# Optimization experiments

Measured on AMD Instinct MI355X. Metric: run time of the kernel, lower is better.

## Reference

```python
import jax, jax.numpy as jnp
import numpy as np

T, H, W, C, HD, K = 4, 128, 128, 256, 8, 9
F = C // HD


def setup_inputs() -> dict:
    key = jax.random.key(0)
    ks = jax.random.split(key, 6)
    x = jax.random.normal(ks[0], (T, H, W, C), jnp.float32)
    attn = jax.random.uniform(ks[1], (1, HD, T, H, W, K), jnp.float32)
    attn = attn / attn.sum(-1, keepdims=True)  # softmax-normalized neighbor weights
    # integer flow offsets (dt, dh, dw) in [-3, 3], as produced by non-local search
    flows = jax.random.randint(ks[2], (1, HD, T, H, W, K, 3), -3, 4, jnp.int32)
    v_w = jax.random.normal(ks[3], (C, C), jnp.float32) * (C ** -0.5)
    proj_w = jax.random.normal(ks[4], (C, C), jnp.float32) * (C ** -0.5)
    proj_b = jnp.zeros((C,), jnp.float32)
    return dict(x=x, attn=attn, flows=flows, v_w=v_w, proj_w=proj_w, proj_b=proj_b)


def reference(x, attn, flows, v_w, proj_w, proj_b):
    T, H, W, C = x.shape
    HD = attn.shape[1]
    F = C // HD
    # v projection, split heads: [T,H,W,HD,F]
    v = (x @ v_w.T).reshape(T, H, W, HD, F)
    fl = flows[0]  # [HD,T,H,W,K,3] integer offsets (dt, dh, dw)
    tt = jnp.clip(jnp.arange(T)[None, :, None, None, None] + fl[..., 0], 0, T - 1)
    hh = jnp.clip(jnp.arange(H)[None, None, :, None, None] + fl[..., 1], 0, H - 1)
    ww = jnp.clip(jnp.arange(W)[None, None, None, :, None] + fl[..., 2], 0, W - 1)
    hd = jnp.arange(HD)[:, None, None, None, None]
    # flow-guided non-local gather: [HD,T,H,W,K,F]
    gathered = v[tt, hh, ww, hd]
    # attention-weighted sum over K neighbors, merge heads: [T,H,W,C]
    out = jnp.einsum('dthwk,dthwkf->thwdf', attn[0], gathered).reshape(T, H, W, C)
    # output projection
    return out @ proj_w.T + proj_b
```

## Files before the change

kernel.cpp:

```cpp
#include <hip/hip_runtime.h>
#include <hip/hip_bf16.h>

namespace {

constexpr int T = 4, H = 128, W = 128, C = 256, HD = 8, K = 9, F = 32;
constexpr int M = T * H * W;

typedef __attribute__((ext_vector_type(8))) short short8v;
typedef __attribute__((ext_vector_type(4))) float f32x4;

__device__ __forceinline__ unsigned short f2bf(float f) {
  unsigned u = __float_as_uint(f);
  unsigned r = (u + 0x7fffu + ((u >> 16) & 1u)) >> 16;
  return (unsigned short)r;
}

__device__ __forceinline__ float bf2f(unsigned short u) {
  return __uint_as_float(((unsigned)u) << 16);
}

template <int ALAYOUT, bool OUT_F32>
__global__ __launch_bounds__(256) void mfma_gemm(
    const void* __restrict__ Aptr, const float* __restrict__ Bw,
    void* __restrict__ Cptr, const float* __restrict__ bias) {
  __shared__ unsigned short As[128][40];
  __shared__ unsigned short Bs[128][40];
  const int m0 = blockIdx.x * 128;
  const int n0 = blockIdx.y * 128;
  const int t = threadIdx.x;
  const int lane = t & 63;
  const int wid = t >> 6;
  const int wm = wid >> 1, wn = wid & 1;
  const int fr = lane & 15;
  const int kg = lane >> 4;

  f32x4 acc[4][4];
#pragma unroll
  for (int ni = 0; ni < 4; ++ni) {
    float b = 0.f;
    if (OUT_F32) b = bias[n0 + wn * 64 + ni * 16 + fr];
#pragma unroll
    for (int mi = 0; mi < 4; ++mi) {
      acc[mi][ni][0] = b; acc[mi][ni][1] = b;
      acc[mi][ni][2] = b; acc[mi][ni][3] = b;
    }
  }

  for (int k0 = 0; k0 < C; k0 += 32) {
    __syncthreads();
    if (ALAYOUT == 2) {
      const unsigned short* Ab = (const unsigned short*)Aptr;
      const size_t hb = (size_t)(k0 >> 5) * M * 32;
#pragma unroll
      for (int i = 0; i < 2; ++i) {
        const int flat = t + i * 256;
        const int row = flat >> 2, kc = (flat & 3) * 8;
        *(short8v*)&As[row][kc] =
            *(const short8v*)(Ab + hb + (size_t)(m0 + row) * 32 + kc);
      }
    } else {
      const float* Af = (const float*)Aptr;
#pragma unroll
      for (int i = 0; i < 4; ++i) {
        const int flat = t + i * 256;
        const int row = flat >> 3, kc = (flat & 7) * 4;
        const float4 v4 = *(const float4*)(Af + (size_t)(m0 + row) * C + k0 + kc);
        ushort4 o;
        o.x = f2bf(v4.x); o.y = f2bf(v4.y); o.z = f2bf(v4.z); o.w = f2bf(v4.w);
        *(ushort4*)&As[row][kc] = o;
      }
    }
#pragma unroll
    for (int i = 0; i < 4; ++i) {
      const int flat = t + i * 256;
      const int row = flat >> 3, kc = (flat & 7) * 4;
      const float4 v4 = *(const float4*)(Bw + (size_t)(n0 + row) * C + k0 + kc);
      ushort4 o;
      o.x = f2bf(v4.x); o.y = f2bf(v4.y); o.z = f2bf(v4.z); o.w = f2bf(v4.w);
      *(ushort4*)&Bs[row][kc] = o;
    }
    __syncthreads();
    short8v af[4], bfv[4];
#pragma unroll
    for (int mi = 0; mi < 4; ++mi)
      af[mi] = *(const short8v*)&As[wm * 64 + mi * 16 + fr][kg * 8];
#pragma unroll
    for (int ni = 0; ni < 4; ++ni)
      bfv[ni] = *(const short8v*)&Bs[wn * 64 + ni * 16 + fr][kg * 8];
#pragma unroll
    for (int mi = 0; mi < 4; ++mi)
#pragma unroll
      for (int ni = 0; ni < 4; ++ni)
        acc[mi][ni] = __builtin_amdgcn_mfma_f32_16x16x32_bf16(
            af[mi], bfv[ni], acc[mi][ni], 0, 0, 0);
  }

#pragma unroll
  for (int mi = 0; mi < 4; ++mi) {
#pragma unroll
    for (int ni = 0; ni < 4; ++ni) {
      const int gcol = n0 + wn * 64 + ni * 16 + fr;
#pragma unroll
      for (int r = 0; r < 4; ++r) {
        const int grow = m0 + wm * 64 + mi * 16 + kg * 4 + r;
        if (OUT_F32) {
          ((float*)Cptr)[(size_t)grow * C + gcol] = acc[mi][ni][r];
        } else {
          ((unsigned short*)Cptr)[(size_t)grow * C + gcol] = f2bf(acc[mi][ni][r]);
        }
      }
    }
  }
}

struct __attribute__((packed, aligned(4))) I4p { int a, b, c, d; };
struct __attribute__((packed, aligned(4))) I2p { int a, b; };
struct __attribute__((packed, aligned(4))) F4p { float a, b, c, d; };

__global__ __launch_bounds__(256, 4) void gather_lds_kernel(
    const unsigned short* __restrict__ v, const float* __restrict__ attn,
    const int* __restrict__ flows, unsigned short* __restrict__ agg2) {
  __shared__ __align__(16) unsigned short halo[4 * 14 * 14 * 32];
  const int nb = (blockIdx.x & 7) * 256 + (blockIdx.x >> 3);
  const int head = nb & 7;
  const int tile = nb >> 3;
  const int h0 = (tile >> 4) * 8;
  const int w0 = (tile & 15) * 8;
  const int tid = threadIdx.x;
  const int s = tid & 63;
  const int tq = tid >> 6;
  const int h = h0 + (s >> 3);
  const int w = w0 + (s & 7);
  const int m = (tq << 14) | (h << 7) | w;

  const int base = ((head << 16) | m) * K;
  const int fb = base * 3;
  const I4p f0 = *(const I4p*)(flows + fb + 0);
  const I4p f1 = *(const I4p*)(flows + fb + 4);
  const I4p f2 = *(const I4p*)(flows + fb + 8);
  const I4p f3 = *(const I4p*)(flows + fb + 12);
  const I4p f4 = *(const I4p*)(flows + fb + 16);
  const I4p f5 = *(const I4p*)(flows + fb + 20);
  const I2p f6 = *(const I2p*)(flows + fb + 24);
  const int f7 = flows[fb + 26];
  const F4p a0 = *(const F4p*)(attn + base + 0);
  const F4p a1 = *(const F4p*)(attn + base + 4);
  const float a2 = attn[base + 8];

  const unsigned short* vhead = v + head * F;
  auto piece_src = [&](int pi, int& ldsoff) -> const short8v* {
    const int sliver = pi >> 2, j = pi & 3;
    const int tt = sliver / 196;
    const int rem = sliver - tt * 196;
    const int hh = rem / 14;
    const int ww = rem - hh * 14;
    const int hc = min(max(h0 - 3 + hh, 0), H - 1);
    const int wc = min(max(w0 - 3 + ww, 0), W - 1);
    const int sm = (tt << 14) | (hc << 7) | wc;
    ldsoff = sliver * 32 + (j ^ (sliver & 3)) * 8;
    return (const short8v*)(vhead + (size_t)sm * C + j * 8);
  };
  {
    short8v pc[7]; int lo[7];
#pragma unroll
    for (int it = 0; it < 7; ++it) pc[it] = *piece_src(tid + it * 256, lo[it]);
#pragma unroll
    for (int it = 0; it < 7; ++it) *(short8v*)&halo[lo[it]] = pc[it];
  }
  {
    short8v pc[5]; int lo[5];
#pragma unroll
    for (int it = 0; it < 5; ++it)
      pc[it] = *piece_src(1792 + tid + it * 256, lo[it]);
    short8v pt; int lot = 0;
    if (tid < 64) pt = *piece_src(3072 + tid, lot);
#pragma unroll
    for (int it = 0; it < 5; ++it) *(short8v*)&halo[lo[it]] = pc[it];
    if (tid < 64) *(short8v*)&halo[lot] = pt;
  }
  __syncthreads();

  const int d[27] = {f0.a, f0.b, f0.c, f0.d, f1.a, f1.b, f1.c, f1.d,
                     f2.a, f2.b, f2.c, f2.d, f3.a, f3.b, f3.c, f3.d,
                     f4.a, f4.b, f4.c, f4.d, f5.a, f5.b, f5.c, f5.d,
                     f6.a, f6.b, f7};
  const float aw[9] = {a0.a, a0.b, a0.c, a0.d, a1.a, a1.b, a1.c, a1.d, a2};
  int row[9];
#pragma unroll
  for (int k = 0; k < 9; ++k) {
    const int ts = min(max(tq + d[3 * k + 0], 0), T - 1);
    const int hs = min(max(h + d[3 * k + 1], 0), H - 1) - (h0 - 3);
    const int ws = min(max(w + d[3 * k + 2], 0), W - 1) - (w0 - 3);
    row[k] = (ts * 14 + hs) * 14 + ws;
  }

  float acc[32];
#pragma unroll
  for (int i = 0; i < 32; ++i) acc[i] = 0.f;
#pragma unroll
  for (int k = 0; k < 9; ++k) {
    const int rbase = row[k] * 32;
    const int rsw = row[k] & 3;
#pragma unroll
    for (int j = 0; j < 4; ++j) {
      const short8v p = *(const short8v*)&halo[rbase + (j ^ rsw) * 8];
#pragma unroll
      for (int e = 0; e < 8; ++e)
        acc[j * 8 + e] += aw[k] * bf2f((unsigned short)p[e]);
    }
  }

  unsigned short* dst = agg2 + ((size_t)head * M + m) * F;
#pragma unroll
  for (int j = 0; j < 4; ++j) {
    short8v o;
#pragma unroll
    for (int e = 0; e < 8; ++e) o[e] = (short)f2bf(acc[j * 8 + e]);
    *(short8v*)(dst + j * 8) = o;
  }
}

__global__ __launch_bounds__(256) void agg_proj_kernel(
    const unsigned short* __restrict__ v, const float* __restrict__ attn,
    const int* __restrict__ flows, const float* __restrict__ proj_w,
    const float* __restrict__ proj_b, float* __restrict__ out) {
  __shared__ float Agg[32][C];
  __shared__ float Bs[32][C];
  const int bid = blockIdx.x;
  const int t = bid >> 9;
  const int h0 = ((bid >> 5) & 15) * 8;
  const int w0 = (bid & 31) * 4;
  const int tid = threadIdx.x;

  const int g = tid >> 3;
  const int f4 = (tid & 7) * 4;
#pragma unroll
  for (int r = 0; r < 8; ++r) {
    const int pi = r * 32 + g;
    const int pos = pi >> 3;
    const int head = pi & 7;
    const int h = h0 + (pos >> 2);
    const int w = w0 + (pos & 3);
    const int base = (((head * T + t) * H + h) * W + w) * K;
    const int fbase = base * 3;
    float4 acc = {0.f, 0.f, 0.f, 0.f};
#pragma unroll
    for (int k = 0; k < K; ++k) {
      const int dt = flows[fbase + k * 3 + 0];
      const int dh = flows[fbase + k * 3 + 1];
      const int dw = flows[fbase + k * 3 + 2];
      const float aw = attn[base + k];
      const int tt = min(max(t + dt, 0), T - 1);
      const int hh = min(max(h + dh, 0), H - 1);
      const int ww = min(max(w + dw, 0), W - 1);
      const int mm = (tt * H + hh) * W + ww;
      const ushort4 r4 = *(const ushort4*)(v + (size_t)mm * C + head * F + f4);
      acc.x += aw * bf2f(r4.x);
      acc.y += aw * bf2f(r4.y);
      acc.z += aw * bf2f(r4.z);
      acc.w += aw * bf2f(r4.w);
    }
    *(float4*)&Agg[pos][head * F + f4] = acc;
  }
  __syncthreads();

  const int tx = tid & 31;
  const int ty = tid >> 5;
  float acc2[4][8];
  {
    const float4 b0 = *(const float4*)(proj_b + tx * 8);
    const float4 b1 = *(const float4*)(proj_b + tx * 8 + 4);
#pragma unroll
    for (int i = 0; i < 4; ++i) {
      acc2[i][0] = b0.x; acc2[i][1] = b0.y; acc2[i][2] = b0.z; acc2[i][3] = b0.w;
      acc2[i][4] = b1.x; acc2[i][5] = b1.y; acc2[i][6] = b1.z; acc2[i][7] = b1.w;
    }
  }
  for (int k0 = 0; k0 < C; k0 += 32) {
#pragma unroll
    for (int i = 0; i < 8; ++i) {
      const float4 w4 = *(const float4*)(proj_w + (size_t)tid * C + k0 + i * 4);
      Bs[i * 4 + 0][tid] = w4.x;
      Bs[i * 4 + 1][tid] = w4.y;
      Bs[i * 4 + 2][tid] = w4.z;
      Bs[i * 4 + 3][tid] = w4.w;
    }
    __syncthreads();
#pragma unroll 4
    for (int kk = 0; kk < 32; ++kk) {
      const float4 bb0 = *(const float4*)&Bs[kk][tx * 8];
      const float4 bb1 = *(const float4*)&Bs[kk][tx * 8 + 4];
      float a[4];
#pragma unroll
      for (int i = 0; i < 4; ++i) a[i] = Agg[ty * 4 + i][k0 + kk];
#pragma unroll
      for (int i = 0; i < 4; ++i) {
        acc2[i][0] += a[i] * bb0.x;
        acc2[i][1] += a[i] * bb0.y;
        acc2[i][2] += a[i] * bb0.z;
        acc2[i][3] += a[i] * bb0.w;
        acc2[i][4] += a[i] * bb1.x;
        acc2[i][5] += a[i] * bb1.y;
        acc2[i][6] += a[i] * bb1.z;
        acc2[i][7] += a[i] * bb1.w;
      }
    }
    __syncthreads();
  }
#pragma unroll
  for (int i = 0; i < 4; ++i) {
    const int pos = ty * 4 + i;
    const int h = h0 + (pos >> 2);
    const int w = w0 + (pos & 3);
    const int m = (t * H + h) * W + w;
    float4 o0, o1;
    o0.x = acc2[i][0]; o0.y = acc2[i][1]; o0.z = acc2[i][2]; o0.w = acc2[i][3];
    o1.x = acc2[i][4]; o1.y = acc2[i][5]; o1.z = acc2[i][6]; o1.w = acc2[i][7];
    *(float4*)(out + (size_t)m * C + tx * 8) = o0;
    *(float4*)(out + (size_t)m * C + tx * 8 + 4) = o1;
  }
}

}

extern "C" void kernel_launch(void* const* d_in, const int* in_sizes, int n_in,
                              void* d_out, int out_size, void* d_ws,
                              size_t ws_size, hipStream_t stream) {
  const float* x = (const float*)d_in[0];
  const float* attn = (const float*)d_in[1];
  const int* flows = (const int*)d_in[2];
  const float* v_w = (const float*)d_in[3];
  const float* proj_w = (const float*)d_in[4];
  const float* proj_b = (const float*)d_in[5];
  float* out = (float*)d_out;

  const size_t VBYTES = (size_t)M * C * 2;
  unsigned short* v = (unsigned short*)d_ws;

  dim3 g1(M / 128, C / 128);
  mfma_gemm<0, false><<<g1, 256, 0, stream>>>(x, v_w, v, nullptr);

  if (ws_size >= 2 * VBYTES) {
    unsigned short* agg2 = (unsigned short*)((char*)d_ws + VBYTES);
    gather_lds_kernel<<<2048, 256, 0, stream>>>(v, attn, flows, agg2);
    mfma_gemm<2, true><<<g1, 256, 0, stream>>>(agg2, proj_w, out, proj_b);
  } else {
    const int nblk = T * (H / 8) * (W / 4);
    agg_proj_kernel<<<nblk, 256, 0, stream>>>(v, attn, flows, proj_w, proj_b,
                                              out);
  }
}
```

Measured before the change: 96.61 us.

## Split gather work over four threads per pixel with smaller 4x4 tiles

The gather kernel now uses 4x4 spatial tiles with a 10x10 halo instead of 8x8 tiles with a 14x14 halo, and launches four times as many blocks. Each output pixel is handled by four threads, each accumulating 8 of the 32 features. Flow and attention loads are split across those four lanes and shared with wave shuffles. This cuts per-thread registers and raises occupancy and parallelism, but the smaller tiles refetch more halo data from global memory per output.

```diff
diff --git a/kernel.cpp b/kernel.cpp
--- a/kernel.cpp
+++ b/kernel.cpp
@@ -114,46 +114,54 @@
 }
 
 struct __attribute__((packed, aligned(4))) I4p { int a, b, c, d; };
-struct __attribute__((packed, aligned(4))) I2p { int a, b; };
 struct __attribute__((packed, aligned(4))) F4p { float a, b, c, d; };
 
-__global__ __launch_bounds__(256, 4) void gather_lds_kernel(
+__global__ __launch_bounds__(256, 6) void gather_lds_kernel(
     const unsigned short* __restrict__ v, const float* __restrict__ attn,
     const int* __restrict__ flows, unsigned short* __restrict__ agg2) {
-  __shared__ __align__(16) unsigned short halo[4 * 14 * 14 * 32];
-  const int nb = (blockIdx.x & 7) * 256 + (blockIdx.x >> 3);
+  __shared__ __align__(16) unsigned short halo[400 * 32];
+  const int nb = (blockIdx.x & 7) * 1024 + (blockIdx.x >> 3);
   const int head = nb & 7;
-  const int tile = nb >> 3;
-  const int h0 = (tile >> 4) * 8;
-  const int w0 = (tile & 15) * 8;
+  const int tcol = (nb >> 3) & 31;
+  const int trow = nb >> 8;
+  const int h0 = trow * 4;
+  const int w0 = tcol * 4;
   const int tid = threadIdx.x;
-  const int s = tid & 63;
-  const int tq = tid >> 6;
-  const int h = h0 + (s >> 3);
-  const int w = w0 + (s & 7);
-  const int m = (tq << 14) | (h << 7) | w;
+  const int o = tid >> 2;
+  const int fq = tid & 3;
+  const int t = o >> 4;
+  const int s = o & 15;
+  const int h = h0 + (s >> 2);
+  const int w = w0 + (s & 3);
+  const int m = (t << 14) | (h << 7) | w;
 
   const int base = ((head << 16) | m) * K;
   const int fb = base * 3;
-  const I4p f0 = *(const I4p*)(flows + fb + 0);
-  const I4p f1 = *(const I4p*)(flows + fb + 4);
-  const I4p f2 = *(const I4p*)(flows + fb + 8);
-  const I4p f3 = *(const I4p*)(flows + fb + 12);
-  const I4p f4 = *(const I4p*)(flows + fb + 16);
-  const I4p f5 = *(const I4p*)(flows + fb + 20);
-  const I2p f6 = *(const I2p*)(flows + fb + 24);
-  const int f7 = flows[fb + 26];
-  const F4p a0 = *(const F4p*)(attn + base + 0);
-  const F4p a1 = *(const F4p*)(attn + base + 4);
-  const float a2 = attn[base + 8];
+  int ld[9];
+  float law[9];
+#pragma unroll
+  for (int i = 0; i < 9; ++i) { ld[i] = 0; law[i] = 0.f; }
+  if (fq < 3) {
+    const I4p g0 = *(const I4p*)(flows + fb + 9 * fq);
+    const I4p g1 = *(const I4p*)(flows + fb + 9 * fq + 4);
+    const int g2 = flows[fb + 9 * fq + 8];
+    ld[0] = g0.a; ld[1] = g0.b; ld[2] = g0.c; ld[3] = g0.d;
+    ld[4] = g1.a; ld[5] = g1.b; ld[6] = g1.c; ld[7] = g1.d; ld[8] = g2;
+  } else {
+    const F4p a0 = *(const F4p*)(attn + base + 0);
+    const F4p a1 = *(const F4p*)(attn + base + 4);
+    const float a2 = attn[base + 8];
+    law[0] = a0.a; law[1] = a0.b; law[2] = a0.c; law[3] = a0.d;
+    law[4] = a1.a; law[5] = a1.b; law[6] = a1.c; law[7] = a1.d; law[8] = a2;
+  }
 
   const unsigned short* vhead = v + head * F;
   auto piece_src = [&](int pi, int& ldsoff) -> const short8v* {
     const int sliver = pi >> 2, j = pi & 3;
-    const int tt = sliver / 196;
-    const int rem = sliver - tt * 196;
-    const int hh = rem / 14;
-    const int ww = rem - hh * 14;
+    const int tt = sliver / 100;
+    const int rem = sliver - tt * 100;
+    const int hh = rem / 10;
+    const int ww = rem - hh * 10;
     const int hc = min(max(h0 - 3 + hh, 0), H - 1);
     const int wc = min(max(w0 - 3 + ww, 0), W - 1);
     const int sm = (tt << 14) | (hc << 7) | wc;
@@ -161,63 +169,56 @@
     return (const short8v*)(vhead + (size_t)sm * C + j * 8);
   };
   {
-    short8v pc[7]; int lo[7];
-#pragma unroll
-    for (int it = 0; it < 7; ++it) pc[it] = *piece_src(tid + it * 256, lo[it]);
-#pragma unroll
-    for (int it = 0; it < 7; ++it) *(short8v*)&halo[lo[it]] = pc[it];
-  }
-  {
-    short8v pc[5]; int lo[5];
-#pragma unroll
-    for (int it = 0; it < 5; ++it)
-      pc[it] = *piece_src(1792 + tid + it * 256, lo[it]);
+    short8v pc[6]; int lo[6];
+#pragma unroll
+    for (int it = 0; it < 6; ++it) pc[it] = *piece_src(tid + it * 256, lo[it]);
     short8v pt; int lot = 0;
-    if (tid < 64) pt = *piece_src(3072 + tid, lot);
-#pragma unroll
-    for (int it = 0; it < 5; ++it) *(short8v*)&halo[lo[it]] = pc[it];
+    if (tid < 64) pt = *piece_src(1536 + tid, lot);
+#pragma unroll
+    for (int it = 0; it < 6; ++it) *(short8v*)&halo[lo[it]] = pc[it];
     if (tid < 64) *(short8v*)&halo[lot] = pt;
   }
+
+  int lrow[3];
+#pragma unroll
+  for (int i = 0; i < 3; ++i) lrow[i] = 0;
+  if (fq < 3) {
+#pragma unroll
+    for (int i = 0; i < 3; ++i) {
+      const int ts = min(max(t + ld[3 * i + 0], 0), T - 1);
+      const int hs = min(max(h + ld[3 * i + 1], 0), H - 1) - (h0 - 3);
+      const int ws = min(max(w + ld[3 * i + 2], 0), W - 1) - (w0 - 3);
+      lrow[i] = (ts * 10 + hs) * 10 + ws;
+    }
+  }
+
+  const int baselane = (tid & 63) & ~3;
+  int row[9]; float aw[9];
+#pragma unroll
+  for (int k = 0; k < 9; ++k) row[k] = __shfl(lrow[k % 3], baselane + k / 3, 64);
+#pragma unroll
+  for (int k = 0; k < 9; ++k) aw[k] = __shfl(law[k], baselane + 3, 64);
+
   __syncthreads();
 
-  const int d[27] = {f0.a, f0.b, f0.c, f0.d, f1.a, f1.b, f1.c, f1.d,
-                     f2.a, f2.b, f2.c, f2.d, f3.a, f3.b, f3.c, f3.d,
-                     f4.a, f4.b, f4.c, f4.d, f5.a, f5.b, f5.c, f5.d,
-                     f6.a, f6.b, f7};
-  const float aw[9] = {a0.a, a0.b, a0.c, a0.d, a1.a, a1.b, a1.c, a1.d, a2};
-  int row[9];
-#pragma unroll
-  for (int k = 0; k < 9; ++k) {
-    const int ts = min(max(tq + d[3 * k + 0], 0), T - 1);
-    const int hs = min(max(h + d[3 * k + 1], 0), H - 1) - (h0 - 3);
-    const int ws = min(max(w + d[3 * k + 2], 0), W - 1) - (w0 - 3);
-    row[k] = (ts * 14 + hs) * 14 + ws;
-  }
-
-  float acc[32];
-#pragma unroll
-  for (int i = 0; i < 32; ++i) acc[i] = 0.f;
+  float acc[8];
+#pragma unroll
+  for (int i = 0; i < 8; ++i) acc[i] = 0.f;
 #pragma unroll
   for (int k = 0; k < 9; ++k) {
     const int rbase = row[k] * 32;
-    const int rsw = row[k] & 3;
-#pragma unroll
-    for (int j = 0; j < 4; ++j) {
-      const short8v p = *(const short8v*)&halo[rbase + (j ^ rsw) * 8];
-#pragma unroll
-      for (int e = 0; e < 8; ++e)
-        acc[j * 8 + e] += aw[k] * bf2f((unsigned short)p[e]);
-    }
-  }
-
-  unsigned short* dst = agg2 + ((size_t)head * M + m) * F;
-#pragma unroll
-  for (int j = 0; j < 4; ++j) {
-    short8v o;
-#pragma unroll
-    for (int e = 0; e < 8; ++e) o[e] = (short)f2bf(acc[j * 8 + e]);
-    *(short8v*)(dst + j * 8) = o;
-  }
+    const int jj = (fq ^ row[k]) & 3;
+    const short8v p = *(const short8v*)&halo[rbase + jj * 8];
+#pragma unroll
+    for (int e = 0; e < 8; ++e)
+      acc[e] += aw[k] * bf2f((unsigned short)p[e]);
+  }
+
+  unsigned short* dst = agg2 + ((size_t)head * M + m) * F + fq * 8;
+  short8v o8;
+#pragma unroll
+  for (int e = 0; e < 8; ++e) o8[e] = (short)f2bf(acc[e]);
+  *(short8v*)dst = o8;
 }
 
 __global__ __launch_bounds__(256) void agg_proj_kernel(
@@ -342,7 +343,7 @@
 
   if (ws_size >= 2 * VBYTES) {
     unsigned short* agg2 = (unsigned short*)((char*)d_ws + VBYTES);
-    gather_lds_kernel<<<2048, 256, 0, stream>>>(v, attn, flows, agg2);
+    gather_lds_kernel<<<8192, 256, 0, stream>>>(v, attn, flows, agg2);
     mfma_gemm<2, true><<<g1, 256, 0, stream>>>(agg2, proj_w, out, proj_b);
   } else {
     const int nblk = T * (H / 8) * (W / 4);
```

Measured after the change: 102.6 us. 1.06x slower.
